# Kernel tuning notes

Measured on AMD Instinct MI355X. Metric: run time of the kernel, lower is better.

The kernel has to match this reference:

```python
import jax, jax.numpy as jnp
import numpy as np

D_MODEL = 2048
M = 128          # compression rate
N_H = 16         # query heads
C = 128          # head dim
D_C = 512        # query compression dim
N_GROUPS = 4
D_G = 512
ROPE_DIM = 64
EPS = 1e-6
B, S = 2, 8192


def _layernorm(x, gamma, beta):
    mu = x.mean(axis=-1, keepdims=True)
    var = ((x - mu) ** 2).mean(axis=-1, keepdims=True)
    return (x - mu) * jax.lax.rsqrt(var + EPS) * gamma + beta


def _partial_rope(q):
    # q: [B,S,H,C]; rotate last ROPE_DIM dims with interleaved complex RoPE
    half = ROPE_DIM // 2
    inv_freq = 1.0 / (10000.0 ** (jnp.arange(0, ROPE_DIM, 2, dtype=jnp.float32) / ROPE_DIM))
    ang = jnp.arange(S, dtype=jnp.float32)[:, None] * inv_freq[None, :]   # [S,half]
    cos = jnp.cos(ang)[None, :, None, :]
    sin = jnp.sin(ang)[None, :, None, :]
    x_part, x_rope = q[..., : C - ROPE_DIM], q[..., C - ROPE_DIM:]
    e, o = x_rope[..., 0::2], x_rope[..., 1::2]
    re = e * cos - o * sin
    ro = e * sin + o * cos
    rot = jnp.stack([re, ro], axis=-1).reshape(*e.shape[:-1], ROPE_DIM)
    return jnp.concatenate([x_part, rot.astype(q.dtype)], axis=-1)


def setup_inputs() -> dict:
    key = jax.random.key(0)
    ks = jax.random.split(key, 12)
    std = 0.02
    inp = {
        "x": jax.random.normal(ks[0], (B, S, D_MODEL), jnp.float32),
        "w_kv": jax.random.normal(ks[1], (D_MODEL, C), jnp.float32) * std,
        "w_z": jax.random.normal(ks[2], (D_MODEL, C), jnp.float32) * std,
        "b_comp": jax.random.normal(ks[3], (M, C), jnp.float32) * std,
        "w_dq": jax.random.normal(ks[4], (D_MODEL, D_C), jnp.float32) * std,
        "w_uq": jax.random.normal(ks[5], (D_C, N_H * C), jnp.float32) * std,
        "o_down_w": jax.random.normal(ks[6], (N_GROUPS, (N_H // N_GROUPS) * C, D_G), jnp.float32) * std,
        "o_up_w": jax.random.normal(ks[7], (N_GROUPS * D_G, D_MODEL), jnp.float32) * std,
        "kv_gamma": jnp.ones((C,), jnp.float32),
        "kv_beta": jnp.zeros((C,), jnp.float32),
        "q_gamma": jnp.ones((C,), jnp.float32),
        "q_beta": jnp.zeros((C,), jnp.float32),
        "sink_logits": jnp.zeros((N_H,), jnp.float32),
    }
    return inp


def reference(x, w_kv, w_z, b_comp, w_dq, w_uq, o_down_w, o_up_w,
              kv_gamma, kv_beta, q_gamma, q_beta, sink_logits):
    n_comp = S // M
    # ---- HeavyCompressor: softmax-weighted pooling per non-overlapping block
    c_proj = x @ w_kv                                     # [B,S,C]
    z = x @ w_z                                           # [B,S,C]
    zb = z.reshape(B, n_comp, M, C) + b_comp              # [B,Nc,M,C]
    w = jax.nn.softmax(zb, axis=2)
    comp = (w * c_proj.reshape(B, n_comp, M, C)).sum(axis=2)   # [B,Nc,C]
    k_comp = _layernorm(comp, kv_gamma, kv_beta)
    v_comp = comp
    # ---- queries: low-rank down/up projection, per-head LN, partial RoPE
    q = (x @ w_dq @ w_uq).reshape(B, S, N_H, C)
    q = _layernorm(q, q_gamma, q_beta)
    q = _partial_rope(q)
    # ---- dense attention over compressed KV with sink-logit denominator
    scores = jnp.einsum("bshc,bkc->bhsk", q.astype(jnp.float32),
                        k_comp.astype(jnp.float32)) / (C ** 0.5)
    allowed = jnp.arange(S)[:, None] >= jnp.arange(n_comp)[None, :] * M  # [S,Nc]
    p = jnp.where(allowed[None, None], jnp.exp(scores), 0.0)
    sink = jnp.exp(sink_logits).reshape(1, N_H, 1, 1)
    attn = p / (p.sum(axis=-1, keepdims=True) + sink)
    out = jnp.einsum("bhsk,bkc->bshc", attn.astype(x.dtype),
                     v_comp.astype(jnp.float32)).astype(x.dtype)
    # ---- grouped output projection
    gsz = N_H // N_GROUPS
    out_g = out.reshape(B, S, N_GROUPS, gsz * C)
    down = jnp.einsum("bsgi,gio->bsgo", out_g, o_down_w).reshape(B, S, N_GROUPS * D_G)
    return down @ o_up_w                                  # [B,S,D_MODEL]
```

## Files before the change

kernel.cpp:

```cpp
#include <hip/hip_runtime.h>
#include <hip/hip_bf16.h>

using bf16 = __hip_bfloat16;
typedef __attribute__((ext_vector_type(8))) short bf16x8;
typedef __attribute__((ext_vector_type(4))) float f32x4;

#define DM 2048

#define OFF_WCZQ  0x00000000ULL
#define OFF_WUQ   0x00300000ULL
#define OFF_DOWNB 0x00500000ULL
#define OFF_WUP   0x00700000ULL
#define OFF_W2T   0x00F00000ULL
#define OFF_KC    0x01700000ULL
#define OFF_VT    0x01710000ULL
#define OFF_ROPE  0x01720000ULL
#define OFF_XB    0x01A00000ULL
#define OFF_CZQ   0x05A00000ULL
#define OFF_QF    0x07300000ULL

__device__ __forceinline__ void async16(const void* g, void* l) {
  __builtin_amdgcn_global_load_lds(
      (const __attribute__((address_space(1))) unsigned int*)g,
      (__attribute__((address_space(3))) unsigned int*)l, 16, 0, 0);
}

__device__ __forceinline__ f32x4 mfma16(bf16x8 a, bf16x8 b, f32x4 c) {
  return __builtin_amdgcn_mfma_f32_16x16x32_bf16(a, b, c, 0, 0, 0);
}

__device__ __forceinline__ float b2f(short u) {
  unsigned x = ((unsigned)(unsigned short)u) << 16;
  return __builtin_bit_cast(float, x);
}
__device__ __forceinline__ short f2bs(float f) {
  return __builtin_bit_cast(short, __float2bfloat16(f));
}

#define SB0 __builtin_amdgcn_sched_barrier(0)

__device__ __forceinline__ void cvt8(const float* __restrict__ in, bf16* __restrict__ out, size_t i) {
  float4 a = *(const float4*)(in + i);
  float4 b = *(const float4*)(in + i + 4);
  struct alignas(16) B8 { bf16 v[8]; } r;
  r.v[0] = __float2bfloat16(a.x); r.v[1] = __float2bfloat16(a.y);
  r.v[2] = __float2bfloat16(a.z); r.v[3] = __float2bfloat16(a.w);
  r.v[4] = __float2bfloat16(b.x); r.v[5] = __float2bfloat16(b.y);
  r.v[6] = __float2bfloat16(b.z); r.v[7] = __float2bfloat16(b.w);
  *(B8*)(out + i) = r;
}

__global__ __launch_bounds__(256) void prep_k(
    const float* __restrict__ w_kv, const float* __restrict__ w_z,
    const float* __restrict__ w_dq, const float* __restrict__ w_uq,
    const float* __restrict__ o_up, const float* __restrict__ o_down,
    const float* __restrict__ x,
    bf16* __restrict__ WCZQ, bf16* __restrict__ WUQ, bf16* __restrict__ WUP,
    bf16* __restrict__ DOWNB, bf16* __restrict__ XB, float2* __restrict__ ROPE) {
  __shared__ float t[32][33];
  const int b = blockIdx.x;
  if (b < 6656) {
    const float* src; bf16* dst; int K, N, tx, ty;
    if (b < 256)       { src = w_kv; dst = WCZQ;              K = 2048; N = 128;  int i = b;        tx = i % 4;  ty = i / 4;  }
    else if (b < 512)  { src = w_z;  dst = WCZQ + 128 * 2048; K = 2048; N = 128;  int i = b - 256;  tx = i % 4;  ty = i / 4;  }
    else if (b < 1536) { src = w_dq; dst = WCZQ + 256 * 2048; K = 2048; N = 512;  int i = b - 512;  tx = i % 16; ty = i / 16; }
    else if (b < 2560) { src = w_uq; dst = WUQ;               K = 512;  N = 2048; int i = b - 1536; tx = i % 64; ty = i / 64; }
    else               { src = o_up; dst = WUP;               K = 2048; N = 2048; int i = b - 2560; tx = i % 64; ty = i / 64; }
    const int tn0 = tx * 32, tk0 = ty * 32;
    const int lx = threadIdx.x & 31, ly = threadIdx.x >> 5;
#pragma unroll
    for (int p = 0; p < 4; p++) {
      int k = tk0 + ly + p * 8, n = tn0 + lx;
      if (k < K && n < N) t[ly + p * 8][lx] = src[(size_t)k * N + n];
    }
    __syncthreads();
#pragma unroll
    for (int p = 0; p < 4; p++) {
      int n = tn0 + ly + p * 8, k = tk0 + lx;
      if (n < N && k < K) dst[(size_t)n * K + k] = __float2bfloat16(t[lx][ly + p * 8]);
    }
  } else if (b < 7168) {
    cvt8(o_down, DOWNB, ((size_t)(b - 6656) * 256 + threadIdx.x) * 8);
  } else if (b < 8192) {
    int idx = (b - 7168) * 256 + threadIdx.x;
    int s = idx >> 5, i = idx & 31;
    double f = pow(10000.0, -((double)(2 * i)) / 64.0);
    double a = (double)s * f;
    ROPE[idx] = make_float2((float)cos(a), (float)sin(a));
  } else {
    cvt8(x, XB, ((size_t)(b - 8192) * 256 + threadIdx.x) * 8);
  }
}

template <int OUT_BF16>
__global__ __launch_bounds__(1024, 1) void gemm8p(
    const bf16* __restrict__ A, int lda,
    const bf16* __restrict__ Bt, int ldb,
    void* __restrict__ Cp, int ldc, int K, int ntiles) {
  __shared__ bf16 lds[2][2][2][256][32];
  const int tid = threadIdx.x;
  const int lane = tid & 63, wid = tid >> 6;
  const int wr = wid >> 2, wc = wid & 3;
  const int wgid = (blockIdx.x & 7) * (gridDim.x >> 3) + (blockIdx.x >> 3);
  const int mt = wgid / ntiles, nt = wgid % ntiles;
  const int srow = tid >> 2;
  const int sunit = (tid & 3) ^ ((tid >> 3) & 3);
  const bf16* gA = A + (size_t)(mt * 256 + srow) * lda + (sunit << 3);
  const bf16* gB = Bt + (size_t)(nt * 256 + srow) * ldb + (sunit << 3);
  char* ldsA = (char*)lds + tid * 16;
  char* ldsB = (char*)lds + 32768 + tid * 16;

#define STAGE_A(dd, h, kc) async16(gA + (kc) + (h) * 32, ldsA + (dd) * 65536 + (h) * 16384)
#define STAGE_B(dd, h, kc) async16(gB + (kc) + (h) * 32, ldsB + (dd) * 65536 + (h) * 16384)

  const int l15 = lane & 15, g = lane >> 4;
  const int gsw = g ^ ((l15 >> 1) & 3);
  const char* ardb = (char*)lds + (size_t)(wr * 64 + l15) * 64 + (gsw << 4);
  const char* brdb = (char*)lds + 32768 + (size_t)(wc * 64 + l15) * 64 + (gsw << 4);

  f32x4 acc[4][4] = {};
  STAGE_A(0, 0, 0); STAGE_B(0, 0, 0); STAGE_A(0, 1, 0); STAGE_B(0, 1, 0);

  const int nkt = K >> 6;
  for (int t = 0; t < nkt; ++t) {
    const int d = t & 1;
    const char* aB = ardb + d * 65536;
    const char* bB = brdb + d * 65536;
    const int kn = (t + 1) << 6;
    const bool pf = (t + 1) < nkt;
    bf16x8 a[4], b0, b1;
    SB0;
    asm volatile("s_waitcnt vmcnt(2)" ::: "memory");
    __builtin_amdgcn_s_barrier();
    asm volatile("" ::: "memory");
    SB0;
    if (pf) STAGE_A(d ^ 1, 0, kn);
#pragma unroll
    for (int m = 0; m < 4; m++) a[m] = *(const bf16x8*)(aB + m * 1024);
    b0 = *(const bf16x8*)(bB);
    b1 = *(const bf16x8*)(bB + 1024);
    __builtin_amdgcn_s_setprio(1);
#pragma unroll
    for (int m = 0; m < 4; m++) {
      acc[m][0] = mfma16(a[m], b0, acc[m][0]);
      acc[m][1] = mfma16(a[m], b1, acc[m][1]);
    }
    __builtin_amdgcn_s_setprio(0);
    if (pf) STAGE_B(d ^ 1, 0, kn);
    b0 = *(const bf16x8*)(bB + 2048);
    b1 = *(const bf16x8*)(bB + 3072);
    __builtin_amdgcn_s_setprio(1);
#pragma unroll
    for (int m = 0; m < 4; m++) {
      acc[m][2] = mfma16(a[m], b0, acc[m][2]);
      acc[m][3] = mfma16(a[m], b1, acc[m][3]);
    }
    __builtin_amdgcn_s_setprio(0);
    SB0;
    if (pf) asm volatile("s_waitcnt vmcnt(2)" ::: "memory");
    else    asm volatile("s_waitcnt vmcnt(0)" ::: "memory");
    __builtin_amdgcn_s_barrier();
    asm volatile("" ::: "memory");
    SB0;
    if (pf) STAGE_A(d ^ 1, 1, kn);
#pragma unroll
    for (int m = 0; m < 4; m++) a[m] = *(const bf16x8*)(aB + 16384 + m * 1024);
    b0 = *(const bf16x8*)(bB + 16384);
    b1 = *(const bf16x8*)(bB + 16384 + 1024);
    __builtin_amdgcn_s_setprio(1);
#pragma unroll
    for (int m = 0; m < 4; m++) {
      acc[m][0] = mfma16(a[m], b0, acc[m][0]);
      acc[m][1] = mfma16(a[m], b1, acc[m][1]);
    }
    __builtin_amdgcn_s_setprio(0);
    if (pf) STAGE_B(d ^ 1, 1, kn);
    b0 = *(const bf16x8*)(bB + 16384 + 2048);
    b1 = *(const bf16x8*)(bB + 16384 + 3072);
    __builtin_amdgcn_s_setprio(1);
#pragma unroll
    for (int m = 0; m < 4; m++) {
      acc[m][2] = mfma16(a[m], b0, acc[m][2]);
      acc[m][3] = mfma16(a[m], b1, acc[m][3]);
    }
    __builtin_amdgcn_s_setprio(0);
  }
#undef STAGE_A
#undef STAGE_B

  const int r4 = (lane >> 4) << 2;
  const size_t row0 = (size_t)mt * 256 + wr * 64;
  const int col0 = nt * 256 + wc * 64;
#pragma unroll
  for (int m = 0; m < 4; m++)
#pragma unroll
    for (int n = 0; n < 4; n++)
#pragma unroll
      for (int j = 0; j < 4; j++) {
        size_t row = row0 + m * 16 + r4 + j;
        size_t col = (size_t)col0 + n * 16 + l15;
        if (OUT_BF16) ((bf16*)Cp)[row * ldc + col] = __float2bfloat16(acc[m][n][j]);
        else          ((float*)Cp)[row * ldc + col] = acc[m][n][j];
      }
}

__global__ __launch_bounds__(256) void gemm_w2t(
    const bf16* __restrict__ WUP, const bf16* __restrict__ DOWNB, bf16* __restrict__ W2T) {
  __shared__ bf16 As[128 * 32];
  __shared__ bf16 Bs[128 * 32];
  const int grp = blockIdx.x >> 6;
  const int inner = blockIdx.x & 63;
  const bf16* A = WUP + grp * 512;
  const bf16* Bt = DOWNB + (size_t)grp * 512 * 512;
  bf16* Cb = W2T + grp * 512;
  const int tid = threadIdx.x;
  const int wave = tid >> 6, lane = tid & 63;
  const int wgid = (inner & 7) * 8 + (inner >> 3);
  const int mt = wgid >> 2, nt = wgid & 3;
  const int srow = tid >> 2, scol = (tid & 3) << 3;
  const bf16* ag = A + (size_t)(mt * 128 + srow) * DM + scol;
  const bf16* bg = Bt + (size_t)(nt * 128 + srow) * 512 + scol;
  char* asw = (char*)As + wave * 1024;
  char* bsw = (char*)Bs + wave * 1024;
  const int l15 = lane & 15, lk = (lane >> 4) << 3;
  const int wm = (wave >> 1) * 64, wn = (wave & 1) * 64;
  f32x4 acc[4][4] = {};
  for (int kt = 0; kt < 512; kt += 32) {
    __syncthreads();
    async16(ag + kt, asw);
    async16(ag + kt + (size_t)64 * DM, asw + 4096);
    async16(bg + kt, bsw);
    async16(bg + kt + (size_t)64 * 512, bsw + 4096);
    __syncthreads();
    bf16x8 af[4], bfr[4];
#pragma unroll
    for (int m = 0; m < 4; m++)
      af[m] = *(const bf16x8*)((const char*)As + (size_t)((wm + m * 16 + l15) * 32 + lk) * 2);
#pragma unroll
    for (int n = 0; n < 4; n++)
      bfr[n] = *(const bf16x8*)((const char*)Bs + (size_t)((wn + n * 16 + l15) * 32 + lk) * 2);
#pragma unroll
    for (int m = 0; m < 4; m++)
#pragma unroll
      for (int n = 0; n < 4; n++)
        acc[m][n] = mfma16(af[m], bfr[n], acc[m][n]);
  }
  const int r4 = (lane >> 4) << 2;
#pragma unroll
  for (int m = 0; m < 4; m++)
#pragma unroll
    for (int n = 0; n < 4; n++)
#pragma unroll
      for (int j = 0; j < 4; j++) {
        size_t row = (size_t)mt * 128 + wm + m * 16 + r4 + j;
        size_t col = (size_t)nt * 128 + wn + n * 16 + l15;
        Cb[row * DM + col] = __float2bfloat16(acc[m][n][j]);
      }
}

__global__ __launch_bounds__(512) void compress_k(
    const bf16* __restrict__ cz, int ldcz, const float* __restrict__ b_comp,
    const float* __restrict__ gamma, const float* __restrict__ beta,
    bf16* __restrict__ k_comp, bf16* __restrict__ vt) {
  const int blk = blockIdx.x;
  const int t = threadIdx.x, c = t & 127, qtr = t >> 7;
  const size_t t0 = (size_t)blk * 128;
  float num = 0.f, den = 0.f;
  for (int m = qtr * 32; m < qtr * 32 + 32; m++) {
    const bf16* r = cz + (t0 + m) * ldcz;
    float w = expf(__bfloat162float(r[128 + c]) + b_comp[m * 128 + c]);
    den += w;
    num += w * __bfloat162float(r[c]);
  }
  __shared__ float sn[4][128], sd[4][128], sv[128];
  sn[qtr][c] = num;
  sd[qtr][c] = den;
  __syncthreads();
  if (qtr == 0)
    sv[c] = (sn[0][c] + sn[1][c] + sn[2][c] + sn[3][c]) /
            (sd[0][c] + sd[1][c] + sd[2][c] + sd[3][c]);
  __syncthreads();
  if (qtr == 0) {
    float v = sv[c];
    float mu = 0.f;
    for (int i = 0; i < 128; i++) mu += sv[i];
    mu *= (1.f / 128.f);
    float var = 0.f;
    for (int i = 0; i < 128; i++) { float d = sv[i] - mu; var += d * d; }
    var *= (1.f / 128.f);
    float kc = (v - mu) * rsqrtf(var + 1e-6f) * gamma[c] + beta[c];
    const int b = blk >> 6, kb = blk & 63;
    k_comp[(size_t)blk * 128 + c] = __float2bfloat16(kc);
    vt[(size_t)b * 8192 + c * 64 + kb] = __float2bfloat16(v);
  }
}

__global__ __launch_bounds__(256) void attn_k(
    const bf16* __restrict__ qln, const bf16* __restrict__ kc,
    const bf16* __restrict__ vt, const float* __restrict__ sink_logits,
    const float* __restrict__ gamma, const float* __restrict__ beta,
    const float2* __restrict__ rope, bf16* __restrict__ out) {
  __shared__ bf16 Qs[128 * 128];
  const int qt = blockIdx.x, hh = blockIdx.y, b = blockIdx.z;
  const int nk = qt + 1;
  const int ntk = (nk + 15) >> 4;
  const int nkk = (nk + 31) >> 5;
  const int tid = threadIdx.x, wave = tid >> 6, lane = tid & 63;
  const int l15 = lane & 15, g = lane >> 4;
  const size_t t0 = (size_t)b * 8192 + (size_t)qt * 128;
  const bf16* kbase = kc + (size_t)b * 64 * 128;
  const bf16* vbase = vt + (size_t)b * 128 * 64;

  {
    const int q = tid >> 1, hf = tid & 1;
    const bf16* gq = qln + (t0 + q) * 2048 + hh * 128 + hf * 64;
    bf16x8 r[8];
#pragma unroll
    for (int i = 0; i < 8; i++) r[i] = *(const bf16x8*)(gq + i * 8);
    float sum = 0.f;
#pragma unroll
    for (int i = 0; i < 8; i++)
#pragma unroll
      for (int j = 0; j < 8; j++) sum += b2f(r[i][j]);
    sum += __shfl_xor(sum, 1);
    const float mu = sum * (1.f / 128.f);
    float var = 0.f;
#pragma unroll
    for (int i = 0; i < 8; i++)
#pragma unroll
      for (int j = 0; j < 8; j++) { float d = b2f(r[i][j]) - mu; var += d * d; }
    var += __shfl_xor(var, 1);
    const float inv = rsqrtf(var * (1.f / 128.f) + 1e-6f);
    const int c0 = hf * 64;
#pragma unroll
    for (int i = 0; i < 8; i++) {
      float y[8];
#pragma unroll
      for (int j = 0; j < 8; j++) {
        int ch = c0 + i * 8 + j;
        y[j] = (b2f(r[i][j]) - mu) * inv * gamma[ch] + beta[ch];
      }
      if (hf) {
#pragma unroll
        for (int j = 0; j < 8; j += 2) {
          float2 cs = rope[((size_t)qt * 128 + q) * 32 + i * 4 + (j >> 1)];
          float e = y[j], o = y[j + 1];
          y[j] = e * cs.x - o * cs.y;
          y[j + 1] = e * cs.y + o * cs.x;
        }
      }
      bf16x8 w;
#pragma unroll
      for (int j = 0; j < 8; j++) w[j] = f2bs(y[j]);
      *(bf16x8*)(Qs + q * 128 + ((hf * 8 + (i ^ (q & 7))) << 3)) = w;
    }
  }
  __syncthreads();

  bf16x8 af[2][4];
#pragma unroll
  for (int m = 0; m < 2; m++) {
    const int q = wave * 32 + m * 16 + l15;
#pragma unroll
    for (int kk = 0; kk < 4; kk++) {
      const int u = (kk * 4 + g) ^ (q & 7);
      af[m][kk] = *(const bf16x8*)(Qs + q * 128 + u * 8);
    }
  }
  __syncthreads();

  f32x4 sacc[2][4] = {};
#pragma unroll
  for (int n = 0; n < 4; n++) {
    if (n < ntk) {
      const bf16* kr = kbase + (n * 16 + l15) * 128 + g * 8;
      bf16x8 b0 = *(const bf16x8*)(kr);
      bf16x8 b1 = *(const bf16x8*)(kr + 32);
      bf16x8 b2 = *(const bf16x8*)(kr + 64);
      bf16x8 b3 = *(const bf16x8*)(kr + 96);
      __builtin_amdgcn_s_setprio(1);
      sacc[0][n] = mfma16(af[0][0], b0, sacc[0][n]);
      sacc[1][n] = mfma16(af[1][0], b0, sacc[1][n]);
      sacc[0][n] = mfma16(af[0][1], b1, sacc[0][n]);
      sacc[1][n] = mfma16(af[1][1], b1, sacc[1][n]);
      sacc[0][n] = mfma16(af[0][2], b2, sacc[0][n]);
      sacc[1][n] = mfma16(af[1][2], b2, sacc[1][n]);
      sacc[0][n] = mfma16(af[0][3], b3, sacc[0][n]);
      sacc[1][n] = mfma16(af[1][3], b3, sacc[1][n]);
      __builtin_amdgcn_s_setprio(0);
    }
  }

  const float sink = expf(sink_logits[hh]);
  const float scale = 0.088388347648318447f;
  bf16* P = Qs;
#pragma unroll
  for (int m = 0; m < 2; m++) {
    float pv[4][4];
    float rs[4] = {0.f, 0.f, 0.f, 0.f};
#pragma unroll
    for (int n = 0; n < 4; n++) {
      int key = n * 16 + l15;
#pragma unroll
      for (int j = 0; j < 4; j++) {
        float p = (key < nk) ? expf(sacc[m][n][j] * scale) : 0.f;
        pv[n][j] = p;
        rs[j] += p;
      }
    }
#pragma unroll
    for (int j = 0; j < 4; j++) {
      float v = rs[j];
      v += __shfl_xor(v, 1); v += __shfl_xor(v, 2);
      v += __shfl_xor(v, 4); v += __shfl_xor(v, 8);
      rs[j] = 1.0f / (v + sink);
    }
    const int row0 = wave * 32 + m * 16 + (g << 2);
#pragma unroll
    for (int n = 0; n < 4; n++)
#pragma unroll
      for (int j = 0; j < 4; j++) {
        int q = row0 + j;
        int k = n * 16 + l15;
        P[q * 64 + ((((k >> 3) ^ (q & 7)) << 3) | (k & 7))] =
            __float2bfloat16(pv[n][j] * rs[j]);
      }
  }

  f32x4 oacc[2][8] = {};
#pragma unroll
  for (int kk = 0; kk < 2; kk++) {
    if (kk < nkk) {
      bf16x8 pa[2];
#pragma unroll
      for (int m = 0; m < 2; m++) {
        const int q = wave * 32 + m * 16 + l15;
        const int u = (kk * 4 + g) ^ (q & 7);
        pa[m] = *(const bf16x8*)(P + q * 64 + u * 8);
      }
#pragma unroll
      for (int n = 0; n < 8; n++) {
        bf16x8 vb = *(const bf16x8*)(vbase + (n * 16 + l15) * 64 + kk * 32 + g * 8);
        __builtin_amdgcn_s_setprio(1);
        oacc[0][n] = mfma16(pa[0], vb, oacc[0][n]);
        oacc[1][n] = mfma16(pa[1], vb, oacc[1][n]);
        __builtin_amdgcn_s_setprio(0);
      }
    }
  }

  bf16* ob = out + t0 * 2048 + hh * 128;
  const int r4 = g << 2;
#pragma unroll
  for (int m = 0; m < 2; m++)
#pragma unroll
    for (int n = 0; n < 8; n++)
#pragma unroll
      for (int j = 0; j < 4; j++)
        ob[(size_t)(wave * 32 + m * 16 + r4 + j) * 2048 + n * 16 + l15] =
            __float2bfloat16(oacc[m][n][j]);
}

extern "C" void kernel_launch(void* const* d_in, const int* in_sizes, int n_in,
                              void* d_out, int out_size, void* d_ws, size_t ws_size,
                              hipStream_t stream) {
  const float* x      = (const float*)d_in[0];
  const float* w_kv   = (const float*)d_in[1];
  const float* w_z    = (const float*)d_in[2];
  const float* b_comp = (const float*)d_in[3];
  const float* w_dq   = (const float*)d_in[4];
  const float* w_uq   = (const float*)d_in[5];
  const float* o_down = (const float*)d_in[6];
  const float* o_up   = (const float*)d_in[7];
  const float* kv_g   = (const float*)d_in[8];
  const float* kv_b   = (const float*)d_in[9];
  const float* q_g    = (const float*)d_in[10];
  const float* q_b    = (const float*)d_in[11];
  const float* sinkl  = (const float*)d_in[12];
  char* ws = (char*)d_ws;
  bf16*   WCZQ  = (bf16*)(ws + OFF_WCZQ);
  bf16*   WUQ   = (bf16*)(ws + OFF_WUQ);
  bf16*   DOWNB = (bf16*)(ws + OFF_DOWNB);
  bf16*   WUP   = (bf16*)(ws + OFF_WUP);
  bf16*   W2T   = (bf16*)(ws + OFF_W2T);
  bf16*   KC    = (bf16*)(ws + OFF_KC);
  bf16*   VT    = (bf16*)(ws + OFF_VT);
  float2* ROPE  = (float2*)(ws + OFF_ROPE);
  bf16*   XB    = (bf16*)(ws + OFF_XB);
  bf16*   CZQ   = (bf16*)(ws + OFF_CZQ);
  bf16*   QF    = (bf16*)(ws + OFF_QF);
  bf16*   ATT   = (bf16*)(ws + OFF_XB);
  float*  OUT   = (float*)d_out;

  prep_k<<<24576, 256, 0, stream>>>(w_kv, w_z, w_dq, w_uq, o_up, o_down, x,
                                    WCZQ, WUQ, WUP, DOWNB, XB, ROPE);
  gemm_w2t<<<256, 256, 0, stream>>>(WUP, DOWNB, W2T);
  gemm8p<1><<<192, 1024, 0, stream>>>(XB, DM, WCZQ, DM, CZQ, 768, DM, 3);
  compress_k<<<128, 512, 0, stream>>>(CZQ, 768, b_comp, kv_g, kv_b, KC, VT);
  gemm8p<1><<<512, 1024, 0, stream>>>(CZQ + 256, 768, WUQ, 512, QF, DM, 512, 8);
  attn_k<<<dim3(64, 16, 2), 256, 0, stream>>>(QF, KC, VT, sinkl, q_g, q_b, ROPE, ATT);
  gemm8p<0><<<512, 1024, 0, stream>>>(ATT, DM, W2T, DM, OUT, DM, DM, 8);
}
```

Before: 377.6 us.

## Fuse W2T weight-product GEMM into the CZQ GEMM launch using shared 256-tile body

Refactors the 256x256 GEMM into a device body and launches one kernel whose first 192 blocks compute the x·[Wkv|Wz|Wdq] product and whose remaining 64 blocks compute the per-group W_up·W_down product. The small 128-tile gemm_w2t kernel is replaced by the same big-tile pipelined body. This removes one launch and fills the 256 CUs, which the 192-block CZQ GEMM previously left partly idle. The W2T blocks have K=512, so they finish earlier than the CZQ blocks and leave some load imbalance.

```diff
diff --git a/kernel.cpp b/kernel.cpp
--- a/kernel.cpp
+++ b/kernel.cpp
@@ -93,30 +93,29 @@
 }
 
 template <int OUT_BF16>
-__global__ __launch_bounds__(1024, 1) void gemm8p(
+__device__ __forceinline__ void gemm8p_body(
+    char* ldsb,
     const bf16* __restrict__ A, int lda,
     const bf16* __restrict__ Bt, int ldb,
-    void* __restrict__ Cp, int ldc, int K, int ntiles) {
-  __shared__ bf16 lds[2][2][2][256][32];
+    void* __restrict__ Cp, int ldc, int K, int ntiles, int wgid) {
   const int tid = threadIdx.x;
   const int lane = tid & 63, wid = tid >> 6;
   const int wr = wid >> 2, wc = wid & 3;
-  const int wgid = (blockIdx.x & 7) * (gridDim.x >> 3) + (blockIdx.x >> 3);
   const int mt = wgid / ntiles, nt = wgid % ntiles;
   const int srow = tid >> 2;
   const int sunit = (tid & 3) ^ ((tid >> 3) & 3);
   const bf16* gA = A + (size_t)(mt * 256 + srow) * lda + (sunit << 3);
   const bf16* gB = Bt + (size_t)(nt * 256 + srow) * ldb + (sunit << 3);
-  char* ldsA = (char*)lds + tid * 16;
-  char* ldsB = (char*)lds + 32768 + tid * 16;
+  char* ldsA = ldsb + tid * 16;
+  char* ldsB = ldsb + 32768 + tid * 16;
 
 #define STAGE_A(dd, h, kc) async16(gA + (kc) + (h) * 32, ldsA + (dd) * 65536 + (h) * 16384)
 #define STAGE_B(dd, h, kc) async16(gB + (kc) + (h) * 32, ldsB + (dd) * 65536 + (h) * 16384)
 
   const int l15 = lane & 15, g = lane >> 4;
   const int gsw = g ^ ((l15 >> 1) & 3);
-  const char* ardb = (char*)lds + (size_t)(wr * 64 + l15) * 64 + (gsw << 4);
-  const char* brdb = (char*)lds + 32768 + (size_t)(wc * 64 + l15) * 64 + (gsw << 4);
+  const char* ardb = ldsb + (size_t)(wr * 64 + l15) * 64 + (gsw << 4);
+  const char* brdb = ldsb + 32768 + (size_t)(wc * 64 + l15) * 64 + (gsw << 4);
 
   f32x4 acc[4][4] = {};
   STAGE_A(0, 0, 0); STAGE_B(0, 0, 0); STAGE_A(0, 1, 0); STAGE_B(0, 1, 0);
@@ -204,58 +203,31 @@
       }
 }
 
-__global__ __launch_bounds__(256) void gemm_w2t(
+template <int OUT_BF16>
+__global__ __launch_bounds__(1024, 1) void gemm8p(
+    const bf16* __restrict__ A, int lda,
+    const bf16* __restrict__ Bt, int ldb,
+    void* __restrict__ Cp, int ldc, int K, int ntiles) {
+  __shared__ __align__(16) char lds[131072];
+  const int wgid = (blockIdx.x & 7) * (gridDim.x >> 3) + (blockIdx.x >> 3);
+  gemm8p_body<OUT_BF16>(lds, A, lda, Bt, ldb, Cp, ldc, K, ntiles, wgid);
+}
+
+__global__ __launch_bounds__(1024, 1) void czq_w2t_k(
+    const bf16* __restrict__ XB, const bf16* __restrict__ WCZQ, bf16* __restrict__ CZQ,
     const bf16* __restrict__ WUP, const bf16* __restrict__ DOWNB, bf16* __restrict__ W2T) {
-  __shared__ bf16 As[128 * 32];
-  __shared__ bf16 Bs[128 * 32];
-  const int grp = blockIdx.x >> 6;
-  const int inner = blockIdx.x & 63;
-  const bf16* A = WUP + grp * 512;
-  const bf16* Bt = DOWNB + (size_t)grp * 512 * 512;
-  bf16* Cb = W2T + grp * 512;
-  const int tid = threadIdx.x;
-  const int wave = tid >> 6, lane = tid & 63;
-  const int wgid = (inner & 7) * 8 + (inner >> 3);
-  const int mt = wgid >> 2, nt = wgid & 3;
-  const int srow = tid >> 2, scol = (tid & 3) << 3;
-  const bf16* ag = A + (size_t)(mt * 128 + srow) * DM + scol;
-  const bf16* bg = Bt + (size_t)(nt * 128 + srow) * 512 + scol;
-  char* asw = (char*)As + wave * 1024;
-  char* bsw = (char*)Bs + wave * 1024;
-  const int l15 = lane & 15, lk = (lane >> 4) << 3;
-  const int wm = (wave >> 1) * 64, wn = (wave & 1) * 64;
-  f32x4 acc[4][4] = {};
-  for (int kt = 0; kt < 512; kt += 32) {
-    __syncthreads();
-    async16(ag + kt, asw);
-    async16(ag + kt + (size_t)64 * DM, asw + 4096);
-    async16(bg + kt, bsw);
-    async16(bg + kt + (size_t)64 * 512, bsw + 4096);
-    __syncthreads();
-    bf16x8 af[4], bfr[4];
-#pragma unroll
-    for (int m = 0; m < 4; m++)
-      af[m] = *(const bf16x8*)((const char*)As + (size_t)((wm + m * 16 + l15) * 32 + lk) * 2);
-#pragma unroll
-    for (int n = 0; n < 4; n++)
-      bfr[n] = *(const bf16x8*)((const char*)Bs + (size_t)((wn + n * 16 + l15) * 32 + lk) * 2);
-#pragma unroll
-    for (int m = 0; m < 4; m++)
-#pragma unroll
-      for (int n = 0; n < 4; n++)
-        acc[m][n] = mfma16(af[m], bfr[n], acc[m][n]);
-  }
-  const int r4 = (lane >> 4) << 2;
-#pragma unroll
-  for (int m = 0; m < 4; m++)
-#pragma unroll
-    for (int n = 0; n < 4; n++)
-#pragma unroll
-      for (int j = 0; j < 4; j++) {
-        size_t row = (size_t)mt * 128 + wm + m * 16 + r4 + j;
-        size_t col = (size_t)nt * 128 + wn + n * 16 + l15;
-        Cb[row * DM + col] = __float2bfloat16(acc[m][n][j]);
-      }
+  __shared__ __align__(16) char lds[131072];
+  const int bx = blockIdx.x;
+  if (bx < 192) {
+    const int wgid = (bx & 7) * 24 + (bx >> 3);
+    gemm8p_body<1>(lds, XB, DM, WCZQ, DM, CZQ, 768, DM, 3, wgid);
+  } else {
+    const int b2 = bx - 192;
+    const int grp = b2 >> 4, inner = b2 & 15;
+    const int wgid = (inner & 7) * 2 + (inner >> 3);
+    gemm8p_body<1>(lds, WUP + grp * 512, DM, DOWNB + (size_t)grp * 512 * 512, 512,
+                   W2T + grp * 512, DM, 512, 2, wgid);
+  }
 }
 
 __global__ __launch_bounds__(512) void compress_k(
@@ -494,8 +466,7 @@
 
   prep_k<<<24576, 256, 0, stream>>>(w_kv, w_z, w_dq, w_uq, o_up, o_down, x,
                                     WCZQ, WUQ, WUP, DOWNB, XB, ROPE);
-  gemm_w2t<<<256, 256, 0, stream>>>(WUP, DOWNB, W2T);
-  gemm8p<1><<<192, 1024, 0, stream>>>(XB, DM, WCZQ, DM, CZQ, 768, DM, 3);
+  czq_w2t_k<<<256, 1024, 0, stream>>>(XB, WCZQ, CZQ, WUP, DOWNB, W2T);
   compress_k<<<128, 512, 0, stream>>>(CZQ, 768, b_comp, kv_g, kv_b, KC, VT);
   gemm8p<1><<<512, 1024, 0, stream>>>(CZQ + 256, 768, WUQ, 512, QF, DM, 512, 8);
   attn_k<<<dim3(64, 16, 2), 256, 0, stream>>>(QF, KC, VT, sinkl, q_g, q_b, ROPE, ATT);
```

Result: faster. 361.9 us (-4.2%).
